# Kernel optimization log

Measured on AMD Instinct MI355X. Metric: run time of the kernel, lower is better.

## Reference

```python
import jax, jax.numpy as jnp
from jax import lax
import numpy as np

W_LAYER = 64   # nodes per layer
N_LAYERS = 64  # number of layers


def _build_graph():
    """Layered lattice DAG: node 0 -> layer1 -> ... -> layerL -> node N-1.
    Returns int64 [E,3] array of (src, dst, gold_bool)."""
    W, L = W_LAYER, N_LAYERS
    layers = 1 + np.arange(L * W, dtype=np.int64).reshape(L, W)
    sink = np.int64(1 + L * W)
    src = np.concatenate([
        np.zeros(W, np.int64),                       # source -> layer 1
        np.repeat(layers[:-1], W, axis=1).ravel(),   # layer l -> layer l+1 (bipartite)
        layers[-1],                                  # layer L -> sink
    ])
    dst = np.concatenate([
        layers[0],
        np.tile(layers[1:], (1, W)).ravel(),
        np.full(W, sink, np.int64),
    ])
    gold = np.random.default_rng(0).integers(0, 2, size=src.shape[0]).astype(np.int64)
    return np.stack([src, dst, gold], axis=1)


def _prep(graph_np):
    """Replicates torch.no_grad() precompute in _get_step_state (all int/structure, no grads)."""
    g = graph_np[:, :2] - graph_np[:, :2].min()
    N = int(g.max()) + 1
    E = g.shape[0]
    dense_idx = np.full((N, N), -1, np.int64)
    dense_idx[g[:, 0], g[:, 1]] = np.arange(E, dtype=np.int64)
    advj = (dense_idx > -1).astype(np.float32)          # [N,N] adjacency
    idegree = advj.sum(0)                               # in-degree per node
    vailed = (idegree != 0).astype(np.float32)
    wmask = np.zeros((N, N), np.float32)
    wmask[(dense_idx + (idegree == 0).astype(np.int64)[None, :]) < 0] = np.inf
    # topological level masks (data-dependent loop on concrete ints)
    flags = np.zeros(N, np.float32)
    flags[0] = 1.0
    masks = []
    while flags.min() < 1:
        passv = flags @ advj
        flags = (passv == idegree).astype(np.float32)
        masks.append(flags * vailed)
    # torch weight[-1] semantics: map -1 -> E-1
    idx_pos = np.where(dense_idx < 0, E - 1, dense_idx)
    return advj, wmask, idx_pos, np.stack(masks, 0), N


def setup_inputs() -> dict:
    graph_np = _build_graph()
    key = jax.random.key(0)
    weight = jax.random.normal(key, (graph_np.shape[0],), dtype=jnp.float32)
    return {"graph": jnp.asarray(graph_np), "weight": weight}


def reference(graph, weight):
    graph_np = np.asarray(graph)
    advj_np, wmask_np, idx_np, masks_np, N = _prep(graph_np)
    advj = jnp.asarray(advj_np)
    wmask = jnp.asarray(wmask_np)
    idx = jnp.asarray(idx_np)
    masks = jnp.asarray(masks_np)  # [L_levels, N]

    gold_score = jnp.sum(weight * graph[:, 2].astype(weight.dtype))
    dense_weight = weight[idx] + wmask  # [N,N], +inf on non-edges

    def step(esum, mask):
        # esum[:,None]*advj zeroes non-edge rows; -inf dense_weight kills them in logsumexp
        new = jax.nn.logsumexp(esum[:, None] * advj - dense_weight, axis=0) * mask
        return new, None

    esum, _ = lax.scan(jax.checkpoint(step), jnp.zeros(N, weight.dtype), masks)
    return gold_score + esum[-1]
```

## Files before the change

### kernel.cpp

```cpp
#include <hip/hip_runtime.h>
#include <hip/hip_bf16.h>
#include <cstdint>


typedef float v2f   __attribute__((ext_vector_type(2)));
typedef float f32x4 __attribute__((ext_vector_type(4)));
typedef unsigned int u32x4 __attribute__((ext_vector_type(4)));

#define NSTEP 16
#define SINK_BASE (64 + 63 * 4096)
#define NGOLD 240
#define LDSTR 68

__global__ __launch_bounds__(256)
void prep_kernel(const int* __restrict__ g, const float* __restrict__ w,
                 unsigned int* __restrict__ wpk, float* __restrict__ partial, int E) {
    const int bid = blockIdx.x, t = threadIdx.x;

    if (bid < 16) {
        __shared__ __align__(16) float Xs[64 * LDSTR];
        __shared__ __align__(16) float Ys[64 * LDSTR];
        __shared__ __align__(16) float Zs[64 * LDSTR];
        const int gg = bid;
        const int L0 = 4 * gg;
        const int ng = (gg == 15) ? 3 : 4;

        {
            const float* src = w + 64 + L0 * 4096;
            #pragma unroll
            for (int j = 0; j < 16; ++j) {
                const int idx = j * 256 + t;
                Xs[(idx >> 6) * LDSTR + (idx & 63)] = __expf(-src[idx]);
            }
        }
        float* cur = Xs;
        float* oth = Zs;
        const int rb = 4 * (t >> 4);
        const int c0 = 4 * (t & 15);

        #pragma unroll 1
        for (int m = 1; m < ng; ++m) {
            const float* src = w + 64 + (L0 + m) * 4096;
            #pragma unroll
            for (int j = 0; j < 16; ++j) {
                const int idx = j * 256 + t;
                Ys[(idx >> 6) * LDSTR + (idx & 63)] = __expf(-src[idx]);
            }
            __syncthreads();
            f32x4 a0 = {0,0,0,0}, a1 = {0,0,0,0}, a2 = {0,0,0,0}, a3 = {0,0,0,0};
            #pragma unroll 4
            for (int k = 0; k < 64; ++k) {
                const f32x4 y = *(const f32x4*)&Ys[k * LDSTR + c0];
                const float x0 = cur[(rb + 0) * LDSTR + k];
                const float x1 = cur[(rb + 1) * LDSTR + k];
                const float x2 = cur[(rb + 2) * LDSTR + k];
                const float x3 = cur[(rb + 3) * LDSTR + k];
                const f32x4 s0 = {x0, x0, x0, x0};
                const f32x4 s1 = {x1, x1, x1, x1};
                const f32x4 s2 = {x2, x2, x2, x2};
                const f32x4 s3 = {x3, x3, x3, x3};
                a0 = __builtin_elementwise_fma(s0, y, a0);
                a1 = __builtin_elementwise_fma(s1, y, a1);
                a2 = __builtin_elementwise_fma(s2, y, a2);
                a3 = __builtin_elementwise_fma(s3, y, a3);
            }
            *(f32x4*)&oth[(rb + 0) * LDSTR + c0] = a0;
            *(f32x4*)&oth[(rb + 1) * LDSTR + c0] = a1;
            *(f32x4*)&oth[(rb + 2) * LDSTR + c0] = a2;
            *(f32x4*)&oth[(rb + 3) * LDSTR + c0] = a3;
            __syncthreads();
            float* tmp = cur; cur = oth; oth = tmp;
        }

        const int kc = (t & 63) >> 4;
        const int bb = 16 * (t >> 6) + (t & 15);
        #pragma unroll
        for (int h = 0; h < 2; ++h) {
            #pragma unroll
            for (int q = 0; q < 4; ++q) {
                const int k = 16 * kc + 2 * (4 * h + q);
                const float x0 = cur[k * LDSTR + bb];
                const float x1 = cur[(k + 1) * LDSTR + bb];
                uint32_t u0 = __float_as_uint(x0); u0 = (u0 + 0x7fffu + ((u0 >> 16) & 1u)) >> 16;
                uint32_t u1 = __float_as_uint(x1); u1 = (u1 + 0x7fffu + ((u1 >> 16) & 1u)) >> 16;
                wpk[gg * 2048 + h * 1024 + t * 4 + q] = u0 | (u1 << 16);
            }
        }
        return;
    }

    const int gid = bid - 16;
    const bool is64 = (g[1] == 0);
    float s = 0.f;
    for (int e = gid * 256 + t; e < E; e += NGOLD * 256) {
        const int idx = 3 * e + 2;
        const int gv = is64 ? g[2 * idx] : g[idx];
        s += w[e] * (float)gv;
    }
    #pragma unroll
    for (int dd = 1; dd < 64; dd <<= 1) s += __shfl_xor(s, dd, 64);
    __shared__ float lsm[4];
    const int wv = t >> 6, ln = t & 63;
    if (ln == 0) lsm[wv] = s;
    __syncthreads();
    if (t == 0) partial[gid] = lsm[0] + lsm[1] + lsm[2] + lsm[3];
}

__global__ __launch_bounds__(256, 1)
void seq_kernel(const float* __restrict__ w, const unsigned int* __restrict__ wpk,
                const float* __restrict__ partial, float* __restrict__ out) {
    __shared__ __align__(16) float ubuf[2][64];
    __shared__ float P[2];
    __shared__ float slds[64];

    const int tid = threadIdx.x;
    const int wv = tid >> 6, l = tid & 63;
    const int kc = l >> 4;
    const int bb = 16 * wv + (l & 15);

    const float z10 = -w[0];
    float LS = z10;
    float uf = __expf(-w[bb] - z10);
    float wsink = w[SINK_BASE + bb];
    float gs = 0.f;
    #pragma unroll
    for (int i = 0; i < 3; ++i) gs += partial[l + (i << 6)];
    if (l < NGOLD - 192) gs += partial[l + 192];
    asm volatile("" : "+v"(LS), "+v"(uf), "+v"(wsink), "+v"(gs));

    if (l < 16) ubuf[0][bb] = uf;
    if (tid == 0) P[0] = 1.0f;

    const uint32_t voff  = (uint32_t)tid * 16u;
    const uint32_t voff2 = voff + 4096u;
    uintptr_t bcur = (uintptr_t)wpk;

    u32x4 q0a, q0b, q1a, q1b, q2a, q2b, q3a, q3b, q4a, q4b;
    u32x4 q5a, q5b, q6a, q6b, q7a, q7b, q8a, q8b, q9a, q9b;

#define LD1(DST, VO)                                                           \
    asm volatile("global_load_dwordx4 %0, %1, %2"                              \
                 : "=v"(DST) : "v"(VO), "s"(bcur))

#define ISSUE(QA, QB) do { LD1(QA, voff); LD1(QB, voff2); bcur += 8192u; } while (0)

#define BAR() do {                                                             \
    asm volatile("s_waitcnt lgkmcnt(0)" ::: "memory");                         \
    __builtin_amdgcn_s_barrier();                                              \
} while (0)

#define BODY(QA, QB, CB, WSTR, DOISS) {                                        \
    const float rho = P[CB];                                                   \
    const f32x4* uqp = (const f32x4*)ubuf[CB];                                 \
    f32x4 uu[4];                                                               \
    uu[0] = uqp[4 * kc + 0];                                                   \
    uu[1] = uqp[4 * kc + 1];                                                   \
    uu[2] = uqp[4 * kc + 2];                                                   \
    uu[3] = uqp[4 * kc + 3];                                                   \
    asm volatile("s_waitcnt vmcnt(" WSTR ")" ::: "memory");                    \
    __builtin_amdgcn_sched_barrier(0);                                         \
    asm volatile("" : "+v"(QA), "+v"(QB));                                     \
    float rc;                                                                  \
    asm("v_rcp_f32 %0, %1" : "=v"(rc) : "v"(rho));                             \
    v2f acc = {0.f, 0.f};                                                      \
    _Pragma("unroll")                                                          \
    for (int m = 0; m < 4; ++m) {                                              \
        _Pragma("unroll")                                                      \
        for (int pp = 0; pp < 2; ++pp) {                                       \
            const int j2 = 2 * m + pp;                                         \
            const unsigned int wd = (j2 < 4) ? QA[j2] : QB[j2 - 4];            \
            v2f wp, up;                                                        \
            wp[0] = __uint_as_float(wd << 16);                                 \
            wp[1] = __uint_as_float(wd & 0xffff0000u);                         \
            up[0] = uu[m][2 * pp]; up[1] = uu[m][2 * pp + 1];                  \
            acc = __builtin_elementwise_fma(wp, up, acc);                      \
        }                                                                      \
    }                                                                          \
    float p = acc[0] + acc[1];                                                 \
    p += __shfl_xor(p, 16, 64);                                                \
    p += __shfl_xor(p, 32, 64);                    \
    uf = p * rc;                                                               \
    if (l < 16) ubuf[(CB) ^ 1][bb] = uf;                                       \
    if (tid == 0) P[(CB) ^ 1] = uf;                                            \
    LS += __logf(rho);                                  \
    if (DOISS) ISSUE(QA, QB);                                                  \
    BAR();                                                                     \
}

    ISSUE(q0a, q0b); ISSUE(q1a, q1b); ISSUE(q2a, q2b); ISSUE(q3a, q3b);
    ISSUE(q4a, q4b); ISSUE(q5a, q5b); ISSUE(q6a, q6b); ISSUE(q7a, q7b);
    ISSUE(q8a, q8b); ISSUE(q9a, q9b);
    BAR();

    BODY(q0a, q0b, 0, "18", 1)
    BODY(q1a, q1b, 1, "18", 1)
    BODY(q2a, q2b, 0, "18", 1)
    BODY(q3a, q3b, 1, "18", 1)
    BODY(q4a, q4b, 0, "18", 1)
    BODY(q5a, q5b, 1, "18", 1)
    BODY(q6a, q6b, 0, "18", 0)
    BODY(q7a, q7b, 1, "16", 0)
    BODY(q8a, q8b, 0, "14", 0)
    BODY(q9a, q9b, 1, "12", 0)
    BODY(q0a, q0b, 0, "10", 0)
    BODY(q1a, q1b, 1, "8",  0)
    BODY(q2a, q2b, 0, "6",  0)
    BODY(q3a, q3b, 1, "4",  0)
    BODY(q4a, q4b, 0, "2",  0)
    BODY(q5a, q5b, 1, "0",  0)

    const float m0 = LS + __logf(uf) - wsink;
    if (l < 16) slds[bb] = m0;
    BAR();

    if (wv == 0) {
        float m = slds[l];
        float s = 1.0f;
        #pragma unroll
        for (int d = 1; d < 64; d <<= 1) {
            const float om = __shfl_xor(m, d, 64);
            const float os = __shfl_xor(s, d, 64);
            const float nm = fmaxf(m, om);
            s = __expf(m - nm) * s + __expf(om - nm) * os;
            m = nm;
        }
        const float vsink = m + __logf(s);
        #pragma unroll
        for (int d = 1; d < 64; d <<= 1) gs += __shfl_xor(gs, d, 64);
        if (l == 0) out[0] = gs + vsink;
    }
}

extern "C" void kernel_launch(void* const* d_in, const int* in_sizes, int n_in,
                              void* d_out, int out_size, void* d_ws, size_t ws_size,
                              hipStream_t stream) {
    const int*   g = (const int*)d_in[0];
    const float* w = (const float*)d_in[1];
    float* out     = (float*)d_out;
    unsigned int* wpk = (unsigned int*)d_ws;
    float* partial = (float*)(wpk + 16 * 2048);
    const int E = in_sizes[0] / 3;

    prep_kernel<<<256, 256, 0, stream>>>(g, w, wpk, partial, E);
    seq_kernel<<<1, 256, 0, stream>>>(w, wpk, partial, out);
}
```

Measured before the change: 22.71 us.

## Prefetch next layer weights into registers during matmul and vectorize LDS X reads

Result: slower. 25.09 us (+10.5%).

```diff
diff --git a/kernel.cpp b/kernel.cpp
--- a/kernel.cpp
+++ b/kernel.cpp
@@ -25,51 +25,75 @@
         const int L0 = 4 * gg;
         const int ng = (gg == 15) ? 3 : 4;
 
+        const int rb = 4 * (t >> 4);
+        const int c0 = 4 * (t & 15);
+
+        float r0[16], r1[16];
         {
-            const float* src = w + 64 + L0 * 4096;
+            const float* s0 = w + 64 + L0 * 4096;
+            const float* s1 = s0 + 4096;
+            #pragma unroll
+            for (int j = 0; j < 16; ++j) r0[j] = s0[j * 256 + t];
+            #pragma unroll
+            for (int j = 0; j < 16; ++j) r1[j] = s1[j * 256 + t];
             #pragma unroll
             for (int j = 0; j < 16; ++j) {
                 const int idx = j * 256 + t;
-                Xs[(idx >> 6) * LDSTR + (idx & 63)] = __expf(-src[idx]);
-            }
-        }
+                Xs[(idx >> 6) * LDSTR + (idx & 63)] = __expf(-r0[j]);
+            }
+            #pragma unroll
+            for (int j = 0; j < 16; ++j) {
+                const int idx = j * 256 + t;
+                Ys[(idx >> 6) * LDSTR + (idx & 63)] = __expf(-r1[j]);
+            }
+        }
+        __syncthreads();
+
         float* cur = Xs;
         float* oth = Zs;
-        const int rb = 4 * (t >> 4);
-        const int c0 = 4 * (t & 15);
+        float rn[16];
 
         #pragma unroll 1
         for (int m = 1; m < ng; ++m) {
-            const float* src = w + 64 + (L0 + m) * 4096;
-            #pragma unroll
-            for (int j = 0; j < 16; ++j) {
-                const int idx = j * 256 + t;
-                Ys[(idx >> 6) * LDSTR + (idx & 63)] = __expf(-src[idx]);
-            }
-            __syncthreads();
+            if (m + 1 < ng) {
+                const float* sn = w + 64 + (L0 + m + 1) * 4096;
+                #pragma unroll
+                for (int j = 0; j < 16; ++j) rn[j] = sn[j * 256 + t];
+            }
             f32x4 a0 = {0,0,0,0}, a1 = {0,0,0,0}, a2 = {0,0,0,0}, a3 = {0,0,0,0};
             #pragma unroll 4
-            for (int k = 0; k < 64; ++k) {
-                const f32x4 y = *(const f32x4*)&Ys[k * LDSTR + c0];
-                const float x0 = cur[(rb + 0) * LDSTR + k];
-                const float x1 = cur[(rb + 1) * LDSTR + k];
-                const float x2 = cur[(rb + 2) * LDSTR + k];
-                const float x3 = cur[(rb + 3) * LDSTR + k];
-                const f32x4 s0 = {x0, x0, x0, x0};
-                const f32x4 s1 = {x1, x1, x1, x1};
-                const f32x4 s2 = {x2, x2, x2, x2};
-                const f32x4 s3 = {x3, x3, x3, x3};
-                a0 = __builtin_elementwise_fma(s0, y, a0);
-                a1 = __builtin_elementwise_fma(s1, y, a1);
-                a2 = __builtin_elementwise_fma(s2, y, a2);
-                a3 = __builtin_elementwise_fma(s3, y, a3);
+            for (int kb = 0; kb < 16; ++kb) {
+                const f32x4 x0 = *(const f32x4*)&cur[(rb + 0) * LDSTR + 4 * kb];
+                const f32x4 x1 = *(const f32x4*)&cur[(rb + 1) * LDSTR + 4 * kb];
+                const f32x4 x2 = *(const f32x4*)&cur[(rb + 2) * LDSTR + 4 * kb];
+                const f32x4 x3 = *(const f32x4*)&cur[(rb + 3) * LDSTR + 4 * kb];
+                #pragma unroll
+                for (int dk = 0; dk < 4; ++dk) {
+                    const f32x4 y = *(const f32x4*)&Ys[(4 * kb + dk) * LDSTR + c0];
+                    const f32x4 s0 = {x0[dk], x0[dk], x0[dk], x0[dk]};
+                    const f32x4 s1 = {x1[dk], x1[dk], x1[dk], x1[dk]};
+                    const f32x4 s2 = {x2[dk], x2[dk], x2[dk], x2[dk]};
+                    const f32x4 s3 = {x3[dk], x3[dk], x3[dk], x3[dk]};
+                    a0 = __builtin_elementwise_fma(s0, y, a0);
+                    a1 = __builtin_elementwise_fma(s1, y, a1);
+                    a2 = __builtin_elementwise_fma(s2, y, a2);
+                    a3 = __builtin_elementwise_fma(s3, y, a3);
+                }
             }
             *(f32x4*)&oth[(rb + 0) * LDSTR + c0] = a0;
             *(f32x4*)&oth[(rb + 1) * LDSTR + c0] = a1;
             *(f32x4*)&oth[(rb + 2) * LDSTR + c0] = a2;
             *(f32x4*)&oth[(rb + 3) * LDSTR + c0] = a3;
             __syncthreads();
-            float* tmp = cur; cur = oth; oth = tmp;
+            if (m + 1 < ng) {
+                #pragma unroll
+                for (int j = 0; j < 16; ++j) {
+                    const int idx = j * 256 + t;
+                    Ys[(idx >> 6) * LDSTR + (idx & 63)] = __expf(-rn[j]);
+                }
+            }
+            { float* tmp = cur; cur = oth; oth = tmp; }
+            __syncthreads();
         }
 
         const int kc = (t & 63) >> 4;
```
